# Kernel tuning notes

Hardware: AMD Instinct MI355X
Metric: run time of the kernel (lower is better)

The kernel has to match this reference:

```python
import jax, jax.numpy as jnp
import numpy as np

NUM_HEADS = 16
HEAD_DIM = 128
WINDOW = 512
ROPE_BASE = 10000.0


def _rope_tables(seq_len, head_dim, dtype=jnp.float32):
    # rotate_dim == head_dim (rope_proportion=1.0)
    inv_freq = 1.0 / (ROPE_BASE ** (jnp.arange(0, head_dim, 2, dtype=jnp.float32) / head_dim))
    freqs = jnp.arange(seq_len, dtype=jnp.float32)[:, None] * inv_freq[None, :]  # (S, D/2)
    return jnp.cos(freqs).astype(dtype), jnp.sin(freqs).astype(dtype)


def _apply_rope(x, cos, sin):
    # x: (B, H, S, D); interleaved-pair RoPE matching torch reference
    x1 = x[..., 0::2]
    x2 = x[..., 1::2]
    cos = cos[None, None]  # (1,1,S,D/2)
    sin = sin[None, None]
    re = x1 * cos - x2 * sin
    ro = x1 * sin + x2 * cos
    out = jnp.stack([re, ro], axis=-1)  # (B,H,S,D/2,2)
    return out.reshape(x.shape)


def setup_inputs() -> dict:
    key = jax.random.key(0)
    ks = jax.random.split(key, 5)
    B, S, D = 2, 2048, 2048
    std = 0.02
    x = jax.random.normal(ks[0], (B, S, D), dtype=jnp.float32)
    Wq = std * jax.random.normal(ks[1], (D, D), dtype=jnp.float32)
    Wk = std * jax.random.normal(ks[2], (D, D), dtype=jnp.float32)
    Wv = std * jax.random.normal(ks[3], (D, D), dtype=jnp.float32)
    Wo = std * jax.random.normal(ks[4], (D, D), dtype=jnp.float32)
    return {"x": x, "Wq": Wq, "Wk": Wk, "Wv": Wv, "Wo": Wo}


def reference(x, Wq, Wk, Wv, Wo):
    B, S, D = x.shape
    H, Dh = NUM_HEADS, HEAD_DIM
    scale = Dh ** -0.5

    def to_heads(t):
        return t.reshape(B, S, H, Dh).transpose(0, 2, 1, 3)  # (B,H,S,Dh)

    q = to_heads(x @ Wq.T)
    k = to_heads(x @ Wk.T)
    v = to_heads(x @ Wv.T)

    cos, sin = _rope_tables(S, Dh)
    q = _apply_rope(q, cos, sin)
    k = _apply_rope(k, cos, sin)

    # sliding-window causal mask: keep if 0 <= row-col < WINDOW
    pos = jnp.arange(S)
    diff = pos[:, None] - pos[None, :]
    keep = (diff >= 0) & (diff < WINDOW)  # (S,S) bool

    scores = jnp.einsum('bhsd,bhtd->bhst', q, k) * scale
    scores = jnp.where(keep[None, None], scores, jnp.finfo(scores.dtype).min)
    attn = jax.nn.softmax(scores, axis=-1)
    out = jnp.einsum('bhst,bhtd->bhsd', attn, v)  # (B,H,S,Dh)
    out = out.transpose(0, 2, 1, 3).reshape(B, S, D)
    return out @ Wo.T
```

## Files before the change

### kernel.cpp

```cpp
#include <hip/hip_runtime.h>
#include <cstdint>
#include <cstddef>

typedef __bf16 bf16x8 __attribute__((ext_vector_type(8)));
typedef float f32x4 __attribute__((ext_vector_type(4)));
typedef float f32x16 __attribute__((ext_vector_type(16)));
typedef unsigned int u32x2v __attribute__((ext_vector_type(2)));
typedef unsigned short u16;

constexpr int S_LEN  = 2048;
constexpr int DMODEL = 2048;
constexpr int NHEAD  = 16;
constexpr int HDIM   = 128;
constexpr int WIN    = 512;

#define AS1 __attribute__((address_space(1)))
#define AS3 __attribute__((address_space(3)))
#define CFENCE asm volatile("" ::: "memory")
#define BAR() do { CFENCE; __builtin_amdgcn_s_barrier(); CFENCE; } while (0)
#define WAITVM(n) asm volatile("s_waitcnt vmcnt(" #n ")" ::: "memory")

__device__ __forceinline__ u16 f2bf(float f) {
  union { float ff; uint32_t u; } a; a.ff = f;
  return (u16)((a.u + 0x7fffu + ((a.u >> 16) & 1u)) >> 16);
}

__device__ __forceinline__ uint32_t cvtpk(float lo, float hi) {
  uint32_t r;
  asm("v_cvt_pk_bf16_f32 %0, %1, %2" : "=v"(r) : "v"(lo), "v"(hi));
  return r;
}

__global__ void cvt_all(const float* __restrict__ x,  const float* __restrict__ wq,
                        const float* __restrict__ wk, const float* __restrict__ wv,
                        const float* __restrict__ wo,
                        u16* __restrict__ xb,  u16* __restrict__ wqb,
                        u16* __restrict__ wkb, u16* __restrict__ wvb,
                        u16* __restrict__ wob) {
  const int total = 6291456;
  int i = blockIdx.x * blockDim.x + threadIdx.x;
  const int stride = gridDim.x * blockDim.x;
  for (; i < total; i += stride) {
    const int r = i >> 20;
    const float* src; u16* dst; int off;
    if (r < 2)       { src = x;  dst = xb;  off = i; }
    else if (r == 2) { src = wq; dst = wqb; off = i - (2 << 20); }
    else if (r == 3) { src = wk; dst = wkb; off = i - (3 << 20); }
    else if (r == 4) { src = wv; dst = wvb; off = i - (4 << 20); }
    else             { src = wo; dst = wob; off = i - (5 << 20); }
    float4 v = reinterpret_cast<const float4*>(src)[off];
    uint2 pk;
    pk.x = (uint32_t)f2bf(v.x) | ((uint32_t)f2bf(v.y) << 16);
    pk.y = (uint32_t)f2bf(v.z) | ((uint32_t)f2bf(v.w) << 16);
    reinterpret_cast<uint2*>(dst)[off] = pk;
  }
}

__global__ void rope_kernel(float* __restrict__ rc, float* __restrict__ rs) {
  const int i = blockIdx.x * blockDim.x + threadIdx.x;
  const int s = i >> 6, f = i & 63;
  const double inv = exp(-(double)f * (log(10000.0) / 64.0));
  const double a = (double)s * inv;
  rc[i] = (float)cos(a);
  rs[i] = (float)sin(a);
}

template<int MODE>
__global__ __launch_bounds__(512, 2)
void gemm256(const u16* __restrict__ A,
             const u16* __restrict__ B0, const u16* __restrict__ B1,
             const u16* __restrict__ B2,
             u16* __restrict__ qout, u16* __restrict__ kout, u16* __restrict__ vtout,
             float* __restrict__ oout,
             const float* __restrict__ rc, const float* __restrict__ rs) {
  constexpr int K = DMODEL;
  constexpr int NK = K / 32;
  constexpr int NF = (MODE == 0) ? 4 : 2;
  constexpr int BSLOT = (MODE == 0) ? 8192 : 4096;
  constexpr int NBL = (MODE == 0) ? 2 : 1;
  __shared__ __align__(16) u16 sm[(MODE == 0) ? 65536 : 49152];

  const int lin = blockIdx.x;
  const int xcd = lin & 7, idx = lin >> 3;
  int mt, ct;
  if constexpr (MODE == 0) { mt = idx & 15; ct = xcd * 3 + (idx >> 4); }
  else                     { mt = idx & 15; ct = xcd * 2 + (idx >> 4); }
  const int region = (MODE == 0) ? (ct >> 3) : 0;
  const u16* Bw = (MODE == 0) ? (region == 0 ? B0 : region == 1 ? B1 : B2) : B0;
  const int brow = mt * 256;
  const int bcoll = (MODE == 0) ? (ct & 7) * 256 : ct * 128;

  const int tid = threadIdx.x;
  const int w = tid >> 6, lane = tid & 63;
  const int lr = lane & 15, lk = lane >> 4;
  const int wm = w >> 2, wn = w & 3;

  const u16* Ag = A  + (size_t)brow * K;
  const u16* Bg = Bw + (size_t)bcoll * K;
  u16* Asl = sm;
  u16* Bsl = sm + 32768;

  f32x4 acc[8][NF] = {};

  auto stageA = [&](int s) {
    u16* slot = Asl + (s & 3) * 8192;
#pragma unroll
    for (int i = 0; i < 2; ++i) {
      const int MF = i * 8 + w;
      const u16* src = Ag + (size_t)(MF * 16 + lr) * K + s * 32 + lk * 8;
      __builtin_amdgcn_global_load_lds((const AS1 void*)src,
          (AS3 void*)(slot + (i * 512 + w * 64) * 8), 16, 0, 0);
    }
  };
  auto stageB = [&](int s) {
    u16* slot = Bsl + (s & 3) * BSLOT;
#pragma unroll
    for (int i = 0; i < NBL; ++i) {
      const int MF = i * 8 + w;
      const u16* src = Bg + (size_t)(MF * 16 + lr) * K + s * 32 + lk * 8;
      __builtin_amdgcn_global_load_lds((const AS1 void*)src,
          (AS3 void*)(slot + (i * 512 + w * 64) * 8), 16, 0, 0);
    }
  };

#pragma unroll
  for (int s = 0; s < 3; ++s) { stageA(s); stageB(s); }
  if constexpr (MODE == 0) WAITVM(8); else WAITVM(6);
  BAR();

  for (int s = 0; s < NK; ++s) {
    const u16* As = Asl + (s & 3) * 8192;
    const u16* Bs = Bsl + (s & 3) * BSLOT;
    bf16x8 afr[4], bfr[NF];
#pragma unroll
    for (int ml = 0; ml < 4; ++ml)
      afr[ml] = *reinterpret_cast<const bf16x8*>(As + ((wm * 8 + ml) * 64 + lk * 16 + lr) * 8);
#pragma unroll
    for (int nf = 0; nf < NF; ++nf)
      bfr[nf] = *reinterpret_cast<const bf16x8*>(Bs + ((wn * NF + nf) * 64 + lk * 16 + lr) * 8);
    if (s + 3 < NK) stageA(s + 3);
    BAR();
    __builtin_amdgcn_s_setprio(1);
#pragma unroll
    for (int ml = 0; ml < 4; ++ml)
#pragma unroll
      for (int nf = 0; nf < NF; ++nf)
        acc[ml][nf] = __builtin_amdgcn_mfma_f32_16x16x32_bf16(afr[ml], bfr[nf], acc[ml][nf], 0, 0, 0);
    __builtin_amdgcn_s_setprio(0);
    BAR();
    bf16x8 afr2[4];
#pragma unroll
    for (int ml = 0; ml < 4; ++ml)
      afr2[ml] = *reinterpret_cast<const bf16x8*>(As + ((wm * 8 + 4 + ml) * 64 + lk * 16 + lr) * 8);
    if (s + 3 < NK) stageB(s + 3);
    BAR();
    __builtin_amdgcn_s_setprio(1);
#pragma unroll
    for (int ml = 0; ml < 4; ++ml)
#pragma unroll
      for (int nf = 0; nf < NF; ++nf)
        acc[4 + ml][nf] = __builtin_amdgcn_mfma_f32_16x16x32_bf16(afr2[ml], bfr[nf], acc[4 + ml][nf], 0, 0, 0);
    __builtin_amdgcn_s_setprio(0);
    if constexpr (MODE == 0) {
      if (s < NK - 3) { WAITVM(8); } else if (s == NK - 3) { WAITVM(4); } else if (s == NK - 2) { WAITVM(0); }
    } else {
      if (s < NK - 3) { WAITVM(6); } else if (s == NK - 3) { WAITVM(3); } else if (s == NK - 2) { WAITVM(0); }
    }
    BAR();
  }

  if constexpr (MODE == 1) {
#pragma unroll
    for (int mf = 0; mf < 8; ++mf) {
      const int gm0 = brow + wm * 128 + mf * 16 + lk * 4;
#pragma unroll
      for (int nf = 0; nf < NF; ++nf) {
        const int gn = bcoll + wn * (16 * NF) + nf * 16 + lr;
#pragma unroll
        for (int j = 0; j < 4; ++j)
          oout[(size_t)(gm0 + j) * DMODEL + gn] = acc[mf][nf][j];
      }
    }
  } else if (region == 2) {
#pragma unroll
    for (int mf = 0; mf < 8; ++mf) {
      const int gm0 = brow + wm * 128 + mf * 16 + lk * 4;
      const int b = gm0 >> 11, s0 = gm0 & 2047;
#pragma unroll
      for (int nf = 0; nf < NF; ++nf) {
        const int gn = bcoll + wn * 64 + nf * 16 + lr;
        const int h = gn >> 7, dh = gn & 127;
        uint2 pk;
        pk.x = (uint32_t)f2bf(acc[mf][nf][0]) | ((uint32_t)f2bf(acc[mf][nf][1]) << 16);
        pk.y = (uint32_t)f2bf(acc[mf][nf][2]) | ((uint32_t)f2bf(acc[mf][nf][3]) << 16);
        *reinterpret_cast<uint2*>(&vtout[((size_t)((b * NHEAD + h) * HDIM + dh)) * S_LEN + s0]) = pk;
      }
    }
  } else {
    u16* QK = region == 0 ? qout : kout;
#pragma unroll
    for (int mf = 0; mf < 8; ++mf) {
      const int gm0 = brow + wm * 128 + mf * 16 + lk * 4;
      const int b = gm0 >> 11, s0 = gm0 & 2047;
#pragma unroll
      for (int nf = 0; nf < NF; ++nf) {
        const int gn = bcoll + wn * 64 + nf * 16 + lr;
        const int h = gn >> 7, dh = gn & 127;
        const int fi = dh >> 1;
        const bool ev = (dh & 1) == 0;
#pragma unroll
        for (int j = 0; j < 4; ++j) {
          float v = acc[mf][nf][j];
          float pp = __shfl_xor(v, 1, 64);
          const float c  = rc[(s0 + j) * 64 + fi];
          const float sn = rs[(s0 + j) * 64 + fi];
          float oo = ev ? (v * c - pp * sn) : (pp * sn + v * c);
          if (region == 0) oo *= 0.08838834764831845f;
          QK[((size_t)(b * NHEAD + h) * S_LEN + (s0 + j)) * HDIM + dh] = f2bf(oo);
        }
      }
    }
  }
}

__global__ __launch_bounds__(256, 2)
void swa3_kernel(const u16* __restrict__ Qp, const u16* __restrict__ Kp,
                 const u16* __restrict__ Vt, u16* __restrict__ AO) {
  __shared__ __align__(16) u16 Ksh[2][64 * 128];
  __shared__ __align__(16) u16 Vsh[2][128 * 64];

  const int lin = blockIdx.x + gridDim.x * blockIdx.y;
  const int slot = lin >> 3;
  const int bh = (lin & 7) * 4 + (slot >> 4);
  const int qt = slot & 15;

  const int w = threadIdx.x >> 6;
  const int lane = threadIdx.x & 63;
  const int lq = lane & 31, hi = lane >> 5;
  const int qb_blk = qt * 128;
  const int qw = qb_blk + w * 32;
  const int qq = qw + lq;

  const u16* Qb = Qp + (size_t)bh * S_LEN * HDIM;
  const u16* Kb = Kp + (size_t)bh * S_LEN * HDIM;
  const u16* Vb = Vt + (size_t)bh * HDIM * S_LEN;

  bf16x8 qf[8];
#pragma unroll
  for (int s = 0; s < 8; ++s)
    qf[s] = *reinterpret_cast<const bf16x8*>(&Qb[(size_t)qq * HDIM + s * 16 + hi * 8]);

  f32x16 ot[4] = {};
  float m = 0.f, lsum = 0.f;

  const int c_lo = (qb_blk >= WIN) ? qb_blk - WIN : 0;
  const int c_hi = qb_blk + 128;

  auto stage = [&](int buf, int kc) {
#pragma unroll
    for (int i = 0; i < 4; ++i) {
      const int u = i * 256 + w * 64 + lane;
      const int row = u >> 4, sl = (u & 15) ^ (row & 7);
      __builtin_amdgcn_global_load_lds(
          (const AS1 void*)(Kb + (size_t)(kc + row) * HDIM + sl * 8),
          (AS3 void*)(&Ksh[buf][(size_t)(i * 256 + w * 64) * 8]), 16, 0, 0);
    }
#pragma unroll
    for (int i = 0; i < 4; ++i) {
      const int u = i * 256 + w * 64 + lane;
      const int row = u >> 3, sl = (u & 7) ^ (row & 7);
      __builtin_amdgcn_global_load_lds(
          (const AS1 void*)(Vb + (size_t)row * S_LEN + kc + sl * 8),
          (AS3 void*)(&Vsh[buf][(size_t)(i * 256 + w * 64) * 8]), 16, 0, 0);
    }
  };

  int buf = 0;
  stage(0, c_lo);
  __syncthreads();

  for (int kc = c_lo; kc < c_hi; kc += 64, buf ^= 1) {
    if (kc + 64 < c_hi) stage(buf ^ 1, kc + 64);

#pragma unroll
    for (int half = 0; half < 2; ++half) {
      const int kch = kc + half * 32;
      if (kch > qw + 31 || kch < qw - 542) continue;

      f32x16 P = {};
#pragma unroll
      for (int s = 0; s < 8; ++s) {
        const int row = half * 32 + lq;
        const int byte = row * 256 + ((s * 32 + hi * 16) ^ ((row & 7) << 4));
        bf16x8 kf = *reinterpret_cast<const bf16x8*>(&Ksh[buf][byte >> 1]);
        P = __builtin_amdgcn_mfma_f32_32x32x16_bf16(kf, qf[s], P, 0, 0, 0);
      }

      const bool needmask = (kch + 32 > qw) || (qw + 31 - kch >= WIN);
      float p[16];
      float pmax = -1e30f;
#pragma unroll
      for (int r = 0; r < 16; ++r) {
        float v = P[r];
        if (needmask) {
          const int kk = kch + (r & 3) + ((r >> 2) << 3) + hi * 4;
          const bool keep = (qq >= kk) && (qq - kk < WIN);
          v = keep ? v : -1e30f;
        }
        p[r] = v;
        pmax = fmaxf(pmax, v);
      }

      if (__any(pmax - m > 8.f)) {
        const float rm = fmaxf(pmax, __shfl_xor(pmax, 32, 64));
        const float mnew = fmaxf(m, rm);
        const float alpha = __expf(m - mnew);
        lsum *= alpha;
#pragma unroll
        for (int dt = 0; dt < 4; ++dt)
#pragma unroll
          for (int r = 0; r < 16; ++r) ot[dt][r] *= alpha;
        m = mnew;
      }

      float ls = 0.f;
#pragma unroll
      for (int r = 0; r < 16; ++r) {
        p[r] = __expf(p[r] - m);
        ls += p[r];
      }
      lsum += ls;

      uint32_t W[8];
#pragma unroll
      for (int i = 0; i < 8; ++i) W[i] = cvtpk(p[2 * i], p[2 * i + 1]);
      u32x2v r02 = __builtin_amdgcn_permlane32_swap(W[0], W[2], false, false);
      u32x2v r13 = __builtin_amdgcn_permlane32_swap(W[1], W[3], false, false);
      u32x2v r46 = __builtin_amdgcn_permlane32_swap(W[4], W[6], false, false);
      u32x2v r57 = __builtin_amdgcn_permlane32_swap(W[5], W[7], false, false);

#pragma unroll
      for (int ks = 0; ks < 2; ++ks) {
        union { uint32_t u[4]; bf16x8 v; } pb;
        if (ks == 0) { pb.u[0] = r02[0]; pb.u[1] = r13[0]; pb.u[2] = r02[1]; pb.u[3] = r13[1]; }
        else         { pb.u[0] = r46[0]; pb.u[1] = r57[0]; pb.u[2] = r46[1]; pb.u[3] = r57[1]; }
#pragma unroll
        for (int dt = 0; dt < 4; ++dt) {
          const int d = dt * 32 + lq;
          const int byte = d * 128 + ((half * 64 + ks * 32 + hi * 16) ^ ((d & 7) << 4));
          bf16x8 vf = *reinterpret_cast<const bf16x8*>(&Vsh[buf][byte >> 1]);
          ot[dt] = __builtin_amdgcn_mfma_f32_32x32x16_bf16(vf, pb.v, ot[dt], 0, 0, 0);
        }
      }
    }
    __syncthreads();
  }

  const float lf = lsum + __shfl_xor(lsum, 32, 64);
  const float inv = 1.f / lf;
  const int b = bh >> 4, h = bh & 15;
  u16* Ob = AO + (size_t)(b * S_LEN + qq) * DMODEL + h * HDIM;
#pragma unroll
  for (int dt = 0; dt < 4; ++dt)
#pragma unroll
    for (int rq = 0; rq < 4; ++rq) {
      uint2 pk;
      pk.x = cvtpk(ot[dt][rq * 4 + 0] * inv, ot[dt][rq * 4 + 1] * inv);
      pk.y = cvtpk(ot[dt][rq * 4 + 2] * inv, ot[dt][rq * 4 + 3] * inv);
      *reinterpret_cast<uint2*>(&Ob[dt * 32 + rq * 8 + hi * 4]) = pk;
    }
}

extern "C" void kernel_launch(void* const* d_in, const int* in_sizes, int n_in,
                              void* d_out, int out_size, void* d_ws, size_t ws_size,
                              hipStream_t stream) {
  const float* x  = (const float*)d_in[0];
  const float* Wq = (const float*)d_in[1];
  const float* Wk = (const float*)d_in[2];
  const float* Wv = (const float*)d_in[3];
  const float* Wo = (const float*)d_in[4];
  float* out = (float*)d_out;

  u16* p = (u16*)d_ws;
  u16* xb  = p; p += (size_t)4096 * 2048;
  u16* wqb = p; p += (size_t)2048 * 2048;
  u16* wkb = p; p += (size_t)2048 * 2048;
  u16* wvb = p; p += (size_t)2048 * 2048;
  u16* wob = p; p += (size_t)2048 * 2048;
  u16* qb  = p; p += (size_t)32 * 2048 * 128;
  u16* kb  = p; p += (size_t)32 * 2048 * 128;
  u16* vtb = p; p += (size_t)32 * 128 * 2048;
  u16* aob = p; p += (size_t)4096 * 2048;
  float* rc = (float*)p;
  float* rs = rc + (size_t)2048 * 64;

  cvt_all<<<3072, 256, 0, stream>>>(x, Wq, Wk, Wv, Wo, xb, wqb, wkb, wvb, wob);
  rope_kernel<<<512, 256, 0, stream>>>(rc, rs);
  gemm256<0><<<384, 512, 0, stream>>>(xb, wqb, wkb, wvb, qb, kb, vtb, nullptr, rc, rs);
  swa3_kernel<<<dim3(16, 32), 256, 0, stream>>>(qb, kb, vtb, aob);
  gemm256<1><<<256, 512, 0, stream>>>(aob, wob, nullptr, nullptr, nullptr, nullptr, nullptr, out, nullptr, nullptr);
}
```

Measured before the change: 253.7 us.

## Replace split-phase 256x256 GEMM with single-phase 256x128 tile GEMM

The QKV projection GEMM drops from 256x256 tiles (384 blocks) to 256x128 tiles (768 blocks on a 48x16 grid). The main loop goes from two half-steps with four barriers to one combined A+B stage and two barriers per k-step. The XCD-aware block swizzle is removed in favour of a plain 2D grid. This cuts barrier count and gives more blocks, at the cost of lower arithmetic intensity per tile and possibly worse L2 locality.

After: 261.9 us. +3.2%, slower.

```diff
diff --git a/kernel.cpp b/kernel.cpp
--- a/kernel.cpp
+++ b/kernel.cpp
@@ -16,8 +16,7 @@
 
 #define AS1 __attribute__((address_space(1)))
 #define AS3 __attribute__((address_space(3)))
-#define CFENCE asm volatile("" ::: "memory")
-#define BAR() do { CFENCE; __builtin_amdgcn_s_barrier(); CFENCE; } while (0)
+#define BAR() do { asm volatile("" ::: "memory"); __builtin_amdgcn_s_barrier(); asm volatile("" ::: "memory"); } while (0)
 #define WAITVM(n) asm volatile("s_waitcnt vmcnt(" #n ")" ::: "memory")
 
 __device__ __forceinline__ u16 f2bf(float f) {
@@ -67,28 +66,21 @@
 
 template<int MODE>
 __global__ __launch_bounds__(512, 2)
-void gemm256(const u16* __restrict__ A,
-             const u16* __restrict__ B0, const u16* __restrict__ B1,
-             const u16* __restrict__ B2,
-             u16* __restrict__ qout, u16* __restrict__ kout, u16* __restrict__ vtout,
-             float* __restrict__ oout,
-             const float* __restrict__ rc, const float* __restrict__ rs) {
+void gemm8p(const u16* __restrict__ A,
+            const u16* __restrict__ B0w, const u16* __restrict__ B1w,
+            const u16* __restrict__ B2w,
+            u16* __restrict__ qout, u16* __restrict__ kout, u16* __restrict__ vtout,
+            float* __restrict__ oout,
+            const float* __restrict__ rc, const float* __restrict__ rs) {
   constexpr int K = DMODEL;
-  constexpr int NK = K / 32;
-  constexpr int NF = (MODE == 0) ? 4 : 2;
-  constexpr int BSLOT = (MODE == 0) ? 8192 : 4096;
-  constexpr int NBL = (MODE == 0) ? 2 : 1;
-  __shared__ __align__(16) u16 sm[(MODE == 0) ? 65536 : 49152];
-
-  const int lin = blockIdx.x;
-  const int xcd = lin & 7, idx = lin >> 3;
-  int mt, ct;
-  if constexpr (MODE == 0) { mt = idx & 15; ct = xcd * 3 + (idx >> 4); }
-  else                     { mt = idx & 15; ct = xcd * 2 + (idx >> 4); }
-  const int region = (MODE == 0) ? (ct >> 3) : 0;
-  const u16* Bw = (MODE == 0) ? (region == 0 ? B0 : region == 1 ? B1 : B2) : B0;
+  constexpr int NH = K / 32;
+  __shared__ __align__(16) u16 sm[4 * 12288];
+
+  const int ct = blockIdx.x, mt = blockIdx.y;
+  const int region = (MODE == 0) ? (ct >> 4) : 0;
+  const u16* Bw = (MODE == 0) ? (region == 0 ? B0w : region == 1 ? B1w : B2w) : B0w;
   const int brow = mt * 256;
-  const int bcoll = (MODE == 0) ? (ct & 7) * 256 : ct * 128;
+  const int bcol = (MODE == 0) ? (ct & 15) * 128 : ct * 128;
 
   const int tid = threadIdx.x;
   const int w = tid >> 6, lane = tid & 63;
@@ -96,76 +88,51 @@
   const int wm = w >> 2, wn = w & 3;
 
   const u16* Ag = A  + (size_t)brow * K;
-  const u16* Bg = Bw + (size_t)bcoll * K;
-  u16* Asl = sm;
-  u16* Bsl = sm + 32768;
-
-  f32x4 acc[8][NF] = {};
-
-  auto stageA = [&](int s) {
-    u16* slot = Asl + (s & 3) * 8192;
+  const u16* Bg = Bw + (size_t)bcol * K;
+
+  f32x4 acc[8][2] = {};
+
+  auto stage = [&](int h) {
+    u16* slot = sm + (h & 3) * 12288;
 #pragma unroll
     for (int i = 0; i < 2; ++i) {
       const int MF = i * 8 + w;
-      const u16* src = Ag + (size_t)(MF * 16 + lr) * K + s * 32 + lk * 8;
+      const u16* src = Ag + (size_t)(MF * 16 + lr) * K + h * 32 + lk * 8;
       __builtin_amdgcn_global_load_lds((const AS1 void*)src,
           (AS3 void*)(slot + (i * 512 + w * 64) * 8), 16, 0, 0);
     }
+    {
+      const u16* src = Bg + (size_t)(w * 16 + lr) * K + h * 32 + lk * 8;
+      __builtin_amdgcn_global_load_lds((const AS1 void*)src,
+          (AS3 void*)(slot + 8192 + (w * 64) * 8), 16, 0, 0);
+    }
   };
-  auto stageB = [&](int s) {
-    u16* slot = Bsl + (s & 3) * BSLOT;
-#pragma unroll
-    for (int i = 0; i < NBL; ++i) {
-      const int MF = i * 8 + w;
-      const u16* src = Bg + (size_t)(MF * 16 + lr) * K + s * 32 + lk * 8;
-      __builtin_amdgcn_global_load_lds((const AS1 void*)src,
-          (AS3 void*)(slot + (i * 512 + w * 64) * 8), 16, 0, 0);
-    }
-  };
-
-#pragma unroll
-  for (int s = 0; s < 3; ++s) { stageA(s); stageB(s); }
-  if constexpr (MODE == 0) WAITVM(8); else WAITVM(6);
+
+  stage(0); stage(1); stage(2);
+  WAITVM(6);
   BAR();
 
-  for (int s = 0; s < NK; ++s) {
-    const u16* As = Asl + (s & 3) * 8192;
-    const u16* Bs = Bsl + (s & 3) * BSLOT;
-    bf16x8 afr[4], bfr[NF];
-#pragma unroll
-    for (int ml = 0; ml < 4; ++ml)
-      afr[ml] = *reinterpret_cast<const bf16x8*>(As + ((wm * 8 + ml) * 64 + lk * 16 + lr) * 8);
-#pragma unroll
-    for (int nf = 0; nf < NF; ++nf)
-      bfr[nf] = *reinterpret_cast<const bf16x8*>(Bs + ((wn * NF + nf) * 64 + lk * 16 + lr) * 8);
-    if (s + 3 < NK) stageA(s + 3);
+  for (int h = 0; h < NH; ++h) {
+    const u16* slot = sm + (h & 3) * 12288;
+    bf16x8 a[8], b[2];
+#pragma unroll
+    for (int mf = 0; mf < 8; ++mf)
+      a[mf] = *reinterpret_cast<const bf16x8*>(slot + (((wm * 8 + mf) * 4 + lk) * 16 + lr) * 8);
+#pragma unroll
+    for (int nf = 0; nf < 2; ++nf)
+      b[nf] = *reinterpret_cast<const bf16x8*>(slot + 8192 + (((wn * 2 + nf) * 4 + lk) * 16 + lr) * 8);
+    if (h + 3 < NH) stage(h + 3);
     BAR();
     __builtin_amdgcn_s_setprio(1);
 #pragma unroll
-    for (int ml = 0; ml < 4; ++ml)
-#pragma unroll
-      for (int nf = 0; nf < NF; ++nf)
-        acc[ml][nf] = __builtin_amdgcn_mfma_f32_16x16x32_bf16(afr[ml], bfr[nf], acc[ml][nf], 0, 0, 0);
+    for (int mf = 0; mf < 8; ++mf)
+#pragma unroll
+      for (int nf = 0; nf < 2; ++nf)
+        acc[mf][nf] = __builtin_amdgcn_mfma_f32_16x16x32_bf16(a[mf], b[nf], acc[mf][nf], 0, 0, 0);
     __builtin_amdgcn_s_setprio(0);
-    BAR();
-    bf16x8 afr2[4];
-#pragma unroll
-    for (int ml = 0; ml < 4; ++ml)
-      afr2[ml] = *reinterpret_cast<const bf16x8*>(As + ((wm * 8 + 4 + ml) * 64 + lk * 16 + lr) * 8);
-    if (s + 3 < NK) stageB(s + 3);
-    BAR();
-    __builtin_amdgcn_s_setprio(1);
-#pragma unroll
-    for (int ml = 0; ml < 4; ++ml)
-#pragma unroll
-      for (int nf = 0; nf < NF; ++nf)
-        acc[4 + ml][nf] = __builtin_amdgcn_mfma_f32_16x16x32_bf16(afr2[ml], bfr[nf], acc[4 + ml][nf], 0, 0, 0);
-    __builtin_amdgcn_s_setprio(0);
-    if constexpr (MODE == 0) {
-      if (s < NK - 3) { WAITVM(8); } else if (s == NK - 3) { WAITVM(4); } else if (s == NK - 2) { WAITVM(0); }
-    } else {
-      if (s < NK - 3) { WAITVM(6); } else if (s == NK - 3) { WAITVM(3); } else if (s == NK - 2) { WAITVM(0); }
-    }
+    if (h < NH - 3)       { WAITVM(6); }
+    else if (h == NH - 3) { WAITVM(3); }
+    else if (h == NH - 2) { WAITVM(0); }
     BAR();
   }
 
@@ -174,8 +141,8 @@
     for (int mf = 0; mf < 8; ++mf) {
       const int gm0 = brow + wm * 128 + mf * 16 + lk * 4;
 #pragma unroll
-      for (int nf = 0; nf < NF; ++nf) {
-        const int gn = bcoll + wn * (16 * NF) + nf * 16 + lr;
+      for (int nf = 0; nf < 2; ++nf) {
+        const int gn = bcol + wn * 32 + nf * 16 + lr;
 #pragma unroll
         for (int j = 0; j < 4; ++j)
           oout[(size_t)(gm0 + j) * DMODEL + gn] = acc[mf][nf][j];
@@ -185,15 +152,15 @@
 #pragma unroll
     for (int mf = 0; mf < 8; ++mf) {
       const int gm0 = brow + wm * 128 + mf * 16 + lk * 4;
-      const int b = gm0 >> 11, s0 = gm0 & 2047;
-#pragma unroll
-      for (int nf = 0; nf < NF; ++nf) {
-        const int gn = bcoll + wn * 64 + nf * 16 + lr;
+      const int b_ = gm0 >> 11, s0 = gm0 & 2047;
+#pragma unroll
+      for (int nf = 0; nf < 2; ++nf) {
+        const int gn = bcol + wn * 32 + nf * 16 + lr;
         const int h = gn >> 7, dh = gn & 127;
         uint2 pk;
         pk.x = (uint32_t)f2bf(acc[mf][nf][0]) | ((uint32_t)f2bf(acc[mf][nf][1]) << 16);
         pk.y = (uint32_t)f2bf(acc[mf][nf][2]) | ((uint32_t)f2bf(acc[mf][nf][3]) << 16);
-        *reinterpret_cast<uint2*>(&vtout[((size_t)((b * NHEAD + h) * HDIM + dh)) * S_LEN + s0]) = pk;
+        *reinterpret_cast<uint2*>(&vtout[((size_t)((b_ * NHEAD + h) * HDIM + dh)) * S_LEN + s0]) = pk;
       }
     }
   } else {
@@ -201,10 +168,10 @@
 #pragma unroll
     for (int mf = 0; mf < 8; ++mf) {
       const int gm0 = brow + wm * 128 + mf * 16 + lk * 4;
-      const int b = gm0 >> 11, s0 = gm0 & 2047;
-#pragma unroll
-      for (int nf = 0; nf < NF; ++nf) {
-        const int gn = bcoll + wn * 64 + nf * 16 + lr;
+      const int b_ = gm0 >> 11, s0 = gm0 & 2047;
+#pragma unroll
+      for (int nf = 0; nf < 2; ++nf) {
+        const int gn = bcol + wn * 32 + nf * 16 + lr;
         const int h = gn >> 7, dh = gn & 127;
         const int fi = dh >> 1;
         const bool ev = (dh & 1) == 0;
@@ -216,7 +183,7 @@
           const float sn = rs[(s0 + j) * 64 + fi];
           float oo = ev ? (v * c - pp * sn) : (pp * sn + v * c);
           if (region == 0) oo *= 0.08838834764831845f;
-          QK[((size_t)(b * NHEAD + h) * S_LEN + (s0 + j)) * HDIM + dh] = f2bf(oo);
+          QK[((size_t)(b_ * NHEAD + h) * S_LEN + (s0 + j)) * HDIM + dh] = f2bf(oo);
         }
       }
     }
@@ -396,7 +363,7 @@
 
   cvt_all<<<3072, 256, 0, stream>>>(x, Wq, Wk, Wv, Wo, xb, wqb, wkb, wvb, wob);
   rope_kernel<<<512, 256, 0, stream>>>(rc, rs);
-  gemm256<0><<<384, 512, 0, stream>>>(xb, wqb, wkb, wvb, qb, kb, vtb, nullptr, rc, rs);
+  gemm8p<0><<<dim3(48, 16), 512, 0, stream>>>(xb, wqb, wkb, wvb, qb, kb, vtb, nullptr, rc, rs);
   swa3_kernel<<<dim3(16, 32), 256, 0, stream>>>(qb, kb, vtb, aob);
-  gemm256<1><<<256, 512, 0, stream>>>(aob, wob, nullptr, nullptr, nullptr, nullptr, nullptr, out, nullptr, nullptr);
-}
+  gemm8p<1><<<dim3(16, 16), 512, 0, stream>>>(aob, wob, nullptr, nullptr, nullptr, nullptr, nullptr, out, nullptr, nullptr);
+}
```
